# Kernel optimization log

Hardware: AMD Instinct MI355X
Metric: run time of the kernel (lower is better)

Reference implementation:

```python
import jax, jax.numpy as jnp
import numpy as np

N_POINTS = 2_000_000
GRID = 256  # voxel grid resolution (D=H=W), production-scale stand-in for source's 128


def setup_inputs() -> dict:
    key = jax.random.key(0)
    k1, k2, k3 = jax.random.split(key, 3)
    coords = jax.random.uniform(k1, (N_POINTS, 3), dtype=jnp.float32,
                                minval=-0.95, maxval=0.95)
    registration_pred = jax.random.normal(k2, (N_POINTS, 3), dtype=jnp.float32) * 0.02
    registration_gt = jax.random.normal(k3, (N_POINTS, 3), dtype=jnp.float32) * 0.02
    return {"registration_pred": registration_pred,
            "registration_gt": registration_gt,
            "coords": coords}


def _splat(pts, size):
    """Trilinear scatter (adjoint of F.grid_sample, align_corners=False,
    zero padding). pts: [N,3] normalized coords in (x,y,z) order mapping to
    (W,H,D). Splats weight 1 per point. Returns [D,H,W] volume."""
    D = H = W = size
    # grid_sample align_corners=False unnormalization: p = ((g+1)*size - 1)/2
    x = ((pts[:, 0] + 1.0) * W - 1.0) * 0.5
    y = ((pts[:, 1] + 1.0) * H - 1.0) * 0.5
    z = ((pts[:, 2] + 1.0) * D - 1.0) * 0.5
    x0f, y0f, z0f = jnp.floor(x), jnp.floor(y), jnp.floor(z)
    fx, fy, fz = x - x0f, y - y0f, z - z0f  # fractional offsets
    x0, y0, z0 = x0f.astype(jnp.int32), y0f.astype(jnp.int32), z0f.astype(jnp.int32)
    vol = jnp.zeros(D * H * W, dtype=pts.dtype)
    for dz in (0, 1):
        wz = fz if dz else (1.0 - fz)
        for dy in (0, 1):
            wy = fy if dy else (1.0 - fy)
            for dx in (0, 1):
                wx = fx if dx else (1.0 - fx)
                xi, yi, zi = x0 + dx, y0 + dy, z0 + dz
                valid = ((xi >= 0) & (xi < W) & (yi >= 0) & (yi < H)
                         & (zi >= 0) & (zi < D))
                w = jnp.where(valid, wx * wy * wz, 0.0)
                idx = jnp.where(valid, (zi * H + yi) * W + xi, 0)
                vol = vol.at[idx].add(w)
    return vol.reshape(D, H, W)


def reference(registration_pred, registration_gt, coords):
    pred_vol = _splat(coords + registration_pred, GRID)
    gt_vol = _splat(coords + registration_gt, GRID)
    # HuberLoss(reduction='sum', delta=1.0)
    d = pred_vol - gt_vol
    ad = jnp.abs(d)
    return jnp.sum(jnp.where(ad <= 1.0, 0.5 * d * d, ad - 0.5))
```

## Files before the change

### kernel.cpp

```cpp
#include <hip/hip_runtime.h>

#define GRID_RES 256
#define NCELLS 1024
#define NB 256
#define BCAP 24576

#define W_SCALE 2097152.0f
#define INV_W (1.0f / 2097152.0f)
#define L_SCALE 512.0f
#define INV_L (1.0f / 512.0f)

template <typename F>
__device__ __forceinline__ void for_each_copy(float px, float py, float pz,
                                              unsigned sign, F&& emit) {
    float x = ((px + 1.0f) * (float)GRID_RES - 1.0f) * 0.5f;
    float y = ((py + 1.0f) * (float)GRID_RES - 1.0f) * 0.5f;
    float z = ((pz + 1.0f) * (float)GRID_RES - 1.0f) * 0.5f;
    float xf = floorf(x), yf = floorf(y), zf = floorf(z);
    int x0 = (int)xf, y0 = (int)yf, z0 = (int)zf;
    unsigned qx = (unsigned)((x - xf) * 65535.0f + 0.5f);
    unsigned qy = (unsigned)((y - yf) * 65535.0f + 0.5f);
    unsigned qz = (unsigned)((z - zf) * 65535.0f + 0.5f);
    unsigned w0 = qx | (qy << 16);

    int cxs[2], cys[2], czs[2];
    int nx = 0, ny = 0, nz = 0;
    {
        bool vA = (x0 >= 0) & (x0 <= 255);
        bool vB = (x0 >= -1) & (x0 <= 254);
        int cA = x0 >> 5, cB = (x0 + 1) >> 5;
        if (vA) cxs[nx++] = cA;
        if (vB && (!vA || cB != cA)) cxs[nx++] = cB;
    }
    {
        bool vA = (y0 >= 0) & (y0 <= 255);
        bool vB = (y0 >= -1) & (y0 <= 254);
        int cA = y0 >> 5, cB = (y0 + 1) >> 5;
        if (vA) cys[ny++] = cA;
        if (vB && (!vA || cB != cA)) cys[ny++] = cB;
    }
    {
        bool vA = (z0 >= 0) & (z0 <= 255);
        bool vB = (z0 >= -1) & (z0 <= 254);
        int cA = z0 >> 4, cB = (z0 + 1) >> 4;
        if (vA) czs[nz++] = cA;
        if (vB && (!vA || cB != cA)) czs[nz++] = cB;
    }
    for (int a = 0; a < nz; ++a) {
        int cz = czs[a];
        unsigned lz = (unsigned)(z0 - (cz << 4) + 1);
        for (int b = 0; b < ny; ++b) {
            int cy = cys[b];
            unsigned ly = (unsigned)(y0 - (cy << 5) + 1);
            for (int c = 0; c < nx; ++c) {
                int cx = cxs[c];
                unsigned lx = (unsigned)(x0 - (cx << 5) + 1);
                int cell = (cz << 6) | (cy << 3) | cx;
                unsigned pack = (lz * 33u + ly) * 33u + lx;
                unsigned w1 = qz | (pack << 16) | (sign << 31);
                emit(cell, w0, w1);
            }
        }
    }
}

__global__ __launch_bounds__(1024) void bin_kernel(
    const float* __restrict__ pred, const float* __restrict__ gt,
    const float* __restrict__ coords, unsigned* __restrict__ segOffT,
    unsigned* __restrict__ segCntT, uint2* __restrict__ payload, int n) {
    __shared__ unsigned h[NCELLS];
    __shared__ unsigned cur[NCELLS];
    __shared__ unsigned wtot[16];
    int b = blockIdx.x;
    int chunk = (n + NB - 1) / NB;
    int start = b * chunk;
    int end = min(start + chunk, n);
    h[threadIdx.x] = 0;
    __syncthreads();

    const float3* c3 = (const float3*)coords;
    const float3* p3 = (const float3*)pred;
    const float3* g3 = (const float3*)gt;

    for (int i = start + (int)threadIdx.x; i < end; i += 1024) {
        float3 c = c3[i];
        float3 p = p3[i];
        float3 g = g3[i];
        for_each_copy(c.x + p.x, c.y + p.y, c.z + p.z, 0u,
                      [&](int cell, unsigned, unsigned) { atomicAdd(&h[cell], 1u); });
        for_each_copy(c.x + g.x, c.y + g.y, c.z + g.z, 1u,
                      [&](int cell, unsigned, unsigned) { atomicAdd(&h[cell], 1u); });
    }
    __syncthreads();

    unsigned x = h[threadIdx.x];
    unsigned incl = x;
    int lane = threadIdx.x & 63, wid = threadIdx.x >> 6;
#pragma unroll
    for (int off = 1; off < 64; off <<= 1) {
        unsigned y = __shfl_up(incl, off, 64);
        if (lane >= off) incl += y;
    }
    if (lane == 63) wtot[wid] = incl;
    __syncthreads();
    if (threadIdx.x == 0) {
        unsigned r = 0;
#pragma unroll
        for (int w = 0; w < 16; ++w) { unsigned v = wtot[w]; wtot[w] = r; r += v; }
    }
    __syncthreads();
    unsigned offE = incl - x + wtot[wid];
    cur[threadIdx.x] = offE;
    segOffT[(size_t)threadIdx.x * NB + b] = offE;
    segCntT[(size_t)threadIdx.x * NB + b] = x;
    __syncthreads();

    uint2* pb = payload + (size_t)b * BCAP;
    for (int i = start + (int)threadIdx.x; i < end; i += 1024) {
        float3 c = c3[i];
        float3 p = p3[i];
        float3 g = g3[i];
        for_each_copy(c.x + p.x, c.y + p.y, c.z + p.z, 0u,
                      [&](int cell, unsigned w0, unsigned w1) {
                          unsigned slot = atomicAdd(&cur[cell], 1u);
                          if (slot < (unsigned)BCAP) pb[slot] = make_uint2(w0, w1);
                      });
        for_each_copy(c.x + g.x, c.y + g.y, c.z + g.z, 1u,
                      [&](int cell, unsigned w0, unsigned w1) {
                          unsigned slot = atomicAdd(&cur[cell], 1u);
                          if (slot < (unsigned)BCAP) pb[slot] = make_uint2(w0, w1);
                      });
    }
}

__global__ __launch_bounds__(1024) void accum_kernel(
    const uint2* __restrict__ payload, const unsigned* __restrict__ segOffT,
    const unsigned* __restrict__ segCntT, int* __restrict__ lossAcc) {
    __shared__ int v[16384];
    __shared__ unsigned sbase[NB + 1];
    __shared__ unsigned pbase[NB];
    __shared__ unsigned w4[4];
    __shared__ float wsum[16];
    int c = blockIdx.x;
    int t = threadIdx.x;
#pragma unroll
    for (int j = 0; j < 16; ++j) v[t + (j << 10)] = 0;

    int lane = t & 63, wid = t >> 6;
    unsigned cnt = 0, off = 0, incl = 0;
    if (t < NB) {
        cnt = segCntT[(size_t)c * NB + t];
        off = segOffT[(size_t)c * NB + t];
        incl = cnt;
#pragma unroll
        for (int o = 1; o < 64; o <<= 1) {
            unsigned y = __shfl_up(incl, o, 64);
            if (lane >= o) incl += y;
        }
        if (lane == 63) w4[wid] = incl;
    }
    __syncthreads();
    if (t == 0) {
        unsigned r = 0;
#pragma unroll
        for (int w = 0; w < 4; ++w) { unsigned q = w4[w]; w4[w] = r; r += q; }
        sbase[NB] = r;
    }
    __syncthreads();
    if (t < NB) {
        sbase[t] = incl - cnt + w4[wid];
        pbase[t] = (unsigned)t * (unsigned)BCAP + off;
    }
    __syncthreads();

    unsigned total = sbase[NB];
    for (unsigned i = t; i < total; i += 1024) {
        int lo = 0, hi = NB - 1;
#pragma unroll
        for (int s = 0; s < 8; ++s) {
            int mid = (lo + hi + 1) >> 1;
            if (sbase[mid] <= i) lo = mid; else hi = mid - 1;
        }
        uint2 p = payload[(size_t)pbase[lo] + (i - sbase[lo])];
        float fx = (float)(p.x & 0xFFFFu) * (1.0f / 65535.0f);
        float fy = (float)(p.x >> 16) * (1.0f / 65535.0f);
        float fz = (float)(p.y & 0xFFFFu) * (1.0f / 65535.0f);
        unsigned pack = (p.y >> 16) & 0x7FFFu;
        unsigned lx = pack % 33u;
        unsigned tt = pack / 33u;
        unsigned ly = tt % 33u;
        unsigned lz = tt / 33u;
        float s = (p.y >> 31) ? -W_SCALE : W_SCALE;
        float wxs[2] = {1.0f - fx, fx};
        float wys[2] = {1.0f - fy, fy};
        float wzs[2] = {1.0f - fz, fz};
        int xb = (int)lx - 1, yb = (int)ly - 1, zb = (int)lz - 1;
#pragma unroll
        for (int dz = 0; dz < 2; ++dz) {
            int rz = zb + dz;
            if ((unsigned)rz > 15u) continue;
            float wz = s * wzs[dz];
#pragma unroll
            for (int dy = 0; dy < 2; ++dy) {
                int ry = yb + dy;
                if ((unsigned)ry > 31u) continue;
                float wyz = wz * wys[dy];
#pragma unroll
                for (int dx = 0; dx < 2; ++dx) {
                    int rx = xb + dx;
                    if ((unsigned)rx > 31u) continue;
                    int iw = __float2int_rn(wyz * wxs[dx]);
                    atomicAdd(&v[(rz << 10) | (ry << 5) | rx], iw);
                }
            }
        }
    }
    __syncthreads();

    float acc = 0.0f;
#pragma unroll
    for (int j = 0; j < 16; ++j) {
        int val = v[t + (j << 10)];
        float d = (float)val * INV_W;
        float ad = fabsf(d);
        acc += (ad <= 1.0f) ? 0.5f * d * d : ad - 0.5f;
    }
#pragma unroll
    for (int o = 32; o > 0; o >>= 1) acc += __shfl_down(acc, o, 64);
    if (lane == 0) wsum[wid] = acc;
    __syncthreads();
    if (t == 0) {
        float tsum = 0.0f;
#pragma unroll
        for (int w = 0; w < 16; ++w) tsum += wsum[w];
        atomicAdd(lossAcc, __float2int_rn(tsum * L_SCALE));
    }
}

__global__ void finalize_kernel(const int* __restrict__ lossAcc,
                                float* __restrict__ out) {
    out[0] = (float)lossAcc[0] * INV_L;
}

extern "C" void kernel_launch(void* const* d_in, const int* in_sizes, int n_in,
                              void* d_out, int out_size, void* d_ws, size_t ws_size,
                              hipStream_t stream) {
    const float* reg_pred = (const float*)d_in[0];
    const float* reg_gt   = (const float*)d_in[1];
    const float* coords   = (const float*)d_in[2];
    float* out = (float*)d_out;

    char* ws = (char*)d_ws;
    int* lossAcc = (int*)ws;
    unsigned* segOffT = (unsigned*)(ws + 256);
    unsigned* segCntT = segOffT + (size_t)NCELLS * NB;
    uint2* payload = (uint2*)((char*)segCntT + (size_t)NCELLS * NB * 4);

    int n = in_sizes[0] / 3;

    hipMemsetAsync(lossAcc, 0, 256, stream);

    bin_kernel<<<NB, 1024, 0, stream>>>(reg_pred, reg_gt, coords, segOffT,
                                        segCntT, payload, n);
    accum_kernel<<<NCELLS, 1024, 0, stream>>>(payload, segOffT, segCntT,
                                              lossAcc);
    finalize_kernel<<<1, 1, 0, stream>>>(lossAcc, out);
}
```

Before: 183.5 us.

## Use 1024 bin blocks with register-cached points and bit-packed payload

The binning kernel now runs with 1024 blocks, and each thread handles at most two points. Each thread computes the per-point voxel info once, keeps it in registers, and reuses it for both the histogram pass and the scatter pass, so inputs are no longer reloaded from global memory. The payload is now packed with plain bit fields: 14-bit z fraction and 6/6/5-bit local offsets. This replaces the div/mod-by-33 decode in the accumulation kernel, at the cost of lower z-weight precision. The loss-accumulator memset moves into the bin kernel, and the accumulation kernel now scans 1024 segment entries per cell with a 10-step binary search. The segment tables and binary search therefore grow.

```diff
diff --git a/kernel.cpp b/kernel.cpp
--- a/kernel.cpp
+++ b/kernel.cpp
@@ -2,17 +2,19 @@
 
 #define GRID_RES 256
 #define NCELLS 1024
-#define NB 256
-#define BCAP 24576
+#define NB 1024
+#define BCAP 6144
+#define NPT 2
 
 #define W_SCALE 2097152.0f
 #define INV_W (1.0f / 2097152.0f)
 #define L_SCALE 512.0f
 #define INV_L (1.0f / 512.0f)
 
-template <typename F>
-__device__ __forceinline__ void for_each_copy(float px, float py, float pz,
-                                              unsigned sign, F&& emit) {
+struct CEv { unsigned w0, w1q, xyz; };
+
+__device__ __forceinline__ CEv make_cev(float px, float py, float pz,
+                                        unsigned sign) {
     float x = ((px + 1.0f) * (float)GRID_RES - 1.0f) * 0.5f;
     float y = ((py + 1.0f) * (float)GRID_RES - 1.0f) * 0.5f;
     float z = ((pz + 1.0f) * (float)GRID_RES - 1.0f) * 0.5f;
@@ -20,9 +22,24 @@
     int x0 = (int)xf, y0 = (int)yf, z0 = (int)zf;
     unsigned qx = (unsigned)((x - xf) * 65535.0f + 0.5f);
     unsigned qy = (unsigned)((y - yf) * 65535.0f + 0.5f);
-    unsigned qz = (unsigned)((z - zf) * 65535.0f + 0.5f);
-    unsigned w0 = qx | (qy << 16);
-
+    unsigned qz = (unsigned)((z - zf) * 16383.0f + 0.5f);
+    bool valid = (x0 >= -1) & (x0 <= 255) & (y0 >= -1) & (y0 <= 255) &
+                 (z0 >= -1) & (z0 <= 255);
+    CEv e;
+    e.w0 = qx | (qy << 16);
+    e.w1q = qz | (sign << 31);
+    e.xyz = valid ? ((unsigned)(x0 + 1) | ((unsigned)(y0 + 1) << 10) |
+                     ((unsigned)(z0 + 1) << 20) | (1u << 30))
+                  : 0u;
+    return e;
+}
+
+template <typename F>
+__device__ __forceinline__ void enum_cells(const CEv& e, F&& emit) {
+    if (!(e.xyz & (1u << 30))) return;
+    int x0 = (int)(e.xyz & 1023u) - 1;
+    int y0 = (int)((e.xyz >> 10) & 1023u) - 1;
+    int z0 = (int)((e.xyz >> 20) & 1023u) - 1;
     int cxs[2], cys[2], czs[2];
     int nx = 0, ny = 0, nz = 0;
     {
@@ -56,9 +73,8 @@
                 int cx = cxs[c];
                 unsigned lx = (unsigned)(x0 - (cx << 5) + 1);
                 int cell = (cz << 6) | (cy << 3) | cx;
-                unsigned pack = (lz * 33u + ly) * 33u + lx;
-                unsigned w1 = qz | (pack << 16) | (sign << 31);
-                emit(cell, w0, w1);
+                unsigned w1 = e.w1q | (lx << 14) | (ly << 20) | (lz << 26);
+                emit(cell, e.w0, w1);
             }
         }
     }
@@ -66,36 +82,50 @@
 
 __global__ __launch_bounds__(1024) void bin_kernel(
     const float* __restrict__ pred, const float* __restrict__ gt,
-    const float* __restrict__ coords, unsigned* __restrict__ segOffT,
-    unsigned* __restrict__ segCntT, uint2* __restrict__ payload, int n) {
+    const float* __restrict__ coords, unsigned* __restrict__ segOff,
+    unsigned* __restrict__ segCnt, uint2* __restrict__ payload,
+    int* __restrict__ lossAcc, int n) {
     __shared__ unsigned h[NCELLS];
-    __shared__ unsigned cur[NCELLS];
     __shared__ unsigned wtot[16];
     int b = blockIdx.x;
+    int t = threadIdx.x;
+    if (b == 0 && t == 0) lossAcc[0] = 0;
+    h[t] = 0;
+    __syncthreads();
+
     int chunk = (n + NB - 1) / NB;
     int start = b * chunk;
     int end = min(start + chunk, n);
-    h[threadIdx.x] = 0;
-    __syncthreads();
-
     const float3* c3 = (const float3*)coords;
     const float3* p3 = (const float3*)pred;
     const float3* g3 = (const float3*)gt;
 
-    for (int i = start + (int)threadIdx.x; i < end; i += 1024) {
-        float3 c = c3[i];
-        float3 p = p3[i];
-        float3 g = g3[i];
-        for_each_copy(c.x + p.x, c.y + p.y, c.z + p.z, 0u,
-                      [&](int cell, unsigned, unsigned) { atomicAdd(&h[cell], 1u); });
-        for_each_copy(c.x + g.x, c.y + g.y, c.z + g.z, 1u,
-                      [&](int cell, unsigned, unsigned) { atomicAdd(&h[cell], 1u); });
-    }
-    __syncthreads();
-
-    unsigned x = h[threadIdx.x];
+    CEv ev[2 * NPT];
+#pragma unroll
+    for (int k = 0; k < NPT; ++k) {
+        int i = start + t + (k << 10);
+        if (i < end) {
+            float3 c = c3[i];
+            float3 p = p3[i];
+            float3 g = g3[i];
+            ev[2 * k] = make_cev(c.x + p.x, c.y + p.y, c.z + p.z, 0u);
+            ev[2 * k + 1] = make_cev(c.x + g.x, c.y + g.y, c.z + g.z, 1u);
+        } else {
+            ev[2 * k].xyz = 0;
+            ev[2 * k + 1].xyz = 0;
+        }
+    }
+
+#pragma unroll
+    for (int k = 0; k < 2 * NPT; ++k)
+        enum_cells(ev[k], [&](int cell, unsigned, unsigned) {
+            atomicAdd(&h[cell], 1u);
+        });
+    __syncthreads();
+
+    unsigned x = h[t];
     unsigned incl = x;
-    int lane = threadIdx.x & 63, wid = threadIdx.x >> 6;
+    int lane = t & 63, wid = t >> 6;
 #pragma unroll
     for (int off = 1; off < 64; off <<= 1) {
         unsigned y = __shfl_up(incl, off, 64);
@@ -103,43 +133,35 @@
     }
     if (lane == 63) wtot[wid] = incl;
     __syncthreads();
-    if (threadIdx.x == 0) {
+    if (t == 0) {
         unsigned r = 0;
 #pragma unroll
         for (int w = 0; w < 16; ++w) { unsigned v = wtot[w]; wtot[w] = r; r += v; }
     }
     __syncthreads();
     unsigned offE = incl - x + wtot[wid];
-    cur[threadIdx.x] = offE;
-    segOffT[(size_t)threadIdx.x * NB + b] = offE;
-    segCntT[(size_t)threadIdx.x * NB + b] = x;
+    segOff[(size_t)b * NCELLS + t] = offE;
+    segCnt[(size_t)b * NCELLS + t] = x;
+    __syncthreads();
+    h[t] = offE;
     __syncthreads();
 
     uint2* pb = payload + (size_t)b * BCAP;
-    for (int i = start + (int)threadIdx.x; i < end; i += 1024) {
-        float3 c = c3[i];
-        float3 p = p3[i];
-        float3 g = g3[i];
-        for_each_copy(c.x + p.x, c.y + p.y, c.z + p.z, 0u,
-                      [&](int cell, unsigned w0, unsigned w1) {
-                          unsigned slot = atomicAdd(&cur[cell], 1u);
-                          if (slot < (unsigned)BCAP) pb[slot] = make_uint2(w0, w1);
-                      });
-        for_each_copy(c.x + g.x, c.y + g.y, c.z + g.z, 1u,
-                      [&](int cell, unsigned w0, unsigned w1) {
-                          unsigned slot = atomicAdd(&cur[cell], 1u);
-                          if (slot < (unsigned)BCAP) pb[slot] = make_uint2(w0, w1);
-                      });
-    }
+#pragma unroll
+    for (int k = 0; k < 2 * NPT; ++k)
+        enum_cells(ev[k], [&](int cell, unsigned w0, unsigned w1) {
+            unsigned slot = atomicAdd(&h[cell], 1u);
+            if (slot < (unsigned)BCAP) pb[slot] = make_uint2(w0, w1);
+        });
 }
 
 __global__ __launch_bounds__(1024) void accum_kernel(
-    const uint2* __restrict__ payload, const unsigned* __restrict__ segOffT,
-    const unsigned* __restrict__ segCntT, int* __restrict__ lossAcc) {
+    const uint2* __restrict__ payload, const unsigned* __restrict__ segOff,
+    const unsigned* __restrict__ segCnt, int* __restrict__ lossAcc) {
     __shared__ int v[16384];
     __shared__ unsigned sbase[NB + 1];
     __shared__ unsigned pbase[NB];
-    __shared__ unsigned w4[4];
+    __shared__ unsigned w16[16];
     __shared__ float wsum[16];
     int c = blockIdx.x;
     int t = threadIdx.x;
@@ -147,54 +169,50 @@
     for (int j = 0; j < 16; ++j) v[t + (j << 10)] = 0;
 
     int lane = t & 63, wid = t >> 6;
-    unsigned cnt = 0, off = 0, incl = 0;
-    if (t < NB) {
-        cnt = segCntT[(size_t)c * NB + t];
-        off = segOffT[(size_t)c * NB + t];
-        incl = cnt;
-#pragma unroll
-        for (int o = 1; o < 64; o <<= 1) {
-            unsigned y = __shfl_up(incl, o, 64);
-            if (lane >= o) incl += y;
-        }
-        if (lane == 63) w4[wid] = incl;
-    }
+    unsigned cnt = segCnt[(size_t)t * NCELLS + c];
+    unsigned off = segOff[(size_t)t * NCELLS + c];
+    unsigned incl = cnt;
+#pragma unroll
+    for (int o = 1; o < 64; o <<= 1) {
+        unsigned y = __shfl_up(incl, o, 64);
+        if (lane >= o) incl += y;
+    }
+    if (lane == 63) w16[wid] = incl;
     __syncthreads();
     if (t == 0) {
         unsigned r = 0;
 #pragma unroll
-        for (int w = 0; w < 4; ++w) { unsigned q = w4[w]; w4[w] = r; r += q; }
+        for (int w = 0; w < 16; ++w) { unsigned q = w16[w]; w16[w] = r; r += q; }
         sbase[NB] = r;
     }
     __syncthreads();
-    if (t < NB) {
-        sbase[t] = incl - cnt + w4[wid];
-        pbase[t] = (unsigned)t * (unsigned)BCAP + off;
-    }
+    if (t == 0) sbase[NB] = w16[15] + incl - cnt + cnt;
+    __syncthreads();
+    sbase[t] = incl - cnt + w16[wid];
+    pbase[t] = (unsigned)t * (unsigned)BCAP + off;
+    if (t == 1023) sbase[NB] = incl + w16[wid];
     __syncthreads();
 
     unsigned total = sbase[NB];
     for (unsigned i = t; i < total; i += 1024) {
         int lo = 0, hi = NB - 1;
 #pragma unroll
-        for (int s = 0; s < 8; ++s) {
+        for (int s = 0; s < 10; ++s) {
             int mid = (lo + hi + 1) >> 1;
             if (sbase[mid] <= i) lo = mid; else hi = mid - 1;
         }
         uint2 p = payload[(size_t)pbase[lo] + (i - sbase[lo])];
         float fx = (float)(p.x & 0xFFFFu) * (1.0f / 65535.0f);
         float fy = (float)(p.x >> 16) * (1.0f / 65535.0f);
-        float fz = (float)(p.y & 0xFFFFu) * (1.0f / 65535.0f);
-        unsigned pack = (p.y >> 16) & 0x7FFFu;
-        unsigned lx = pack % 33u;
-        unsigned tt = pack / 33u;
-        unsigned ly = tt % 33u;
-        unsigned lz = tt / 33u;
+        float fz = (float)(p.y & 0x3FFFu) * (1.0f / 16383.0f);
+        int lx = (int)((p.y >> 14) & 63u);
+        int ly = (int)((p.y >> 20) & 63u);
+        int lz = (int)((p.y >> 26) & 31u);
         float s = (p.y >> 31) ? -W_SCALE : W_SCALE;
         float wxs[2] = {1.0f - fx, fx};
         float wys[2] = {1.0f - fy, fy};
         float wzs[2] = {1.0f - fz, fz};
-        int xb = (int)lx - 1, yb = (int)ly - 1, zb = (int)lz - 1;
+        int xb = lx - 1, yb = ly - 1, zb = lz - 1;
 #pragma unroll
         for (int dz = 0; dz < 2; ++dz) {
             int rz = zb + dz;
@@ -252,17 +270,15 @@
 
     char* ws = (char*)d_ws;
     int* lossAcc = (int*)ws;
-    unsigned* segOffT = (unsigned*)(ws + 256);
-    unsigned* segCntT = segOffT + (size_t)NCELLS * NB;
-    uint2* payload = (uint2*)((char*)segCntT + (size_t)NCELLS * NB * 4);
+    unsigned* segOff = (unsigned*)(ws + 256);
+    unsigned* segCnt = segOff + (size_t)NB * NCELLS;
+    uint2* payload = (uint2*)((char*)segCnt + (size_t)NB * NCELLS * 4);
 
     int n = in_sizes[0] / 3;
 
-    hipMemsetAsync(lossAcc, 0, 256, stream);
-
-    bin_kernel<<<NB, 1024, 0, stream>>>(reg_pred, reg_gt, coords, segOffT,
-                                        segCntT, payload, n);
-    accum_kernel<<<NCELLS, 1024, 0, stream>>>(payload, segOffT, segCntT,
+    bin_kernel<<<NB, 1024, 0, stream>>>(reg_pred, reg_gt, coords, segOff,
+                                        segCnt, payload, lossAcc, n);
+    accum_kernel<<<NCELLS, 1024, 0, stream>>>(payload, segOff, segCnt,
                                               lossAcc);
     finalize_kernel<<<1, 1, 0, stream>>>(lossAcc, out);
 }
```

Result: faster. 167.2 us (-8.9%).
